# Kernel tuning notes

Measured on AMD Instinct MI355X. Metric: run time of the kernel, lower is better.

The kernel has to match this reference:

```python
import jax, jax.numpy as jnp
import numpy as np

N = 100000   # nodes
E = 800000   # edges
D = 64       # feature dim (input=hidden=output)
EPS = 1e-5   # BatchNorm eps


def setup_inputs() -> dict:
    key = jax.random.key(0)
    ks = jax.random.split(key, 24)
    s = 1.0 / np.sqrt(D)
    inp = {
        "x": jax.random.normal(ks[0], (N, D), jnp.float32),
        "edge_index": jax.random.randint(ks[1], (2, E), 0, N, jnp.int64),
        # GCNConv weights (x @ W + b after normalized aggregation)
        "W1": jax.random.normal(ks[2], (D, D), jnp.float32) * s,
        "b1": jax.random.normal(ks[3], (D,), jnp.float32) * 0.01,
        "W2": jax.random.normal(ks[4], (D, D), jnp.float32) * s,
        "b2": jax.random.normal(ks[5], (D,), jnp.float32) * 0.01,
        "W3": jax.random.normal(ks[6], (D, D), jnp.float32) * s,
        "b3": jax.random.normal(ks[7], (D,), jnp.float32) * 0.01,
        # BatchNorm1d (inference: running stats)
        "bn1_g": jax.random.uniform(ks[8], (D,), jnp.float32, 0.5, 1.5),
        "bn1_b": jax.random.normal(ks[9], (D,), jnp.float32) * 0.1,
        "bn1_m": jax.random.normal(ks[10], (D,), jnp.float32) * 0.1,
        "bn1_v": jax.random.uniform(ks[11], (D,), jnp.float32, 0.5, 1.5),
        "bn2_g": jax.random.uniform(ks[12], (D,), jnp.float32, 0.5, 1.5),
        "bn2_b": jax.random.normal(ks[13], (D,), jnp.float32) * 0.1,
        "bn2_m": jax.random.normal(ks[14], (D,), jnp.float32) * 0.1,
        "bn2_v": jax.random.uniform(ks[15], (D,), jnp.float32, 0.5, 1.5),
        # predictor MLP: Linear -> tanh -> (dropout=id) -> Linear
        "pW1": jax.random.normal(ks[16], (D, D), jnp.float32) * s,
        "pb1": jax.random.normal(ks[17], (D,), jnp.float32) * 0.01,
        "pW2": jax.random.normal(ks[18], (D, D), jnp.float32) * s,
        "pb2": jax.random.normal(ks[19], (D,), jnp.float32) * 0.01,
    }
    return inp


def _gcn_norm(edge_index):
    # add self loops, compute sym-normalized edge coefficients (PyG GCNConv)
    loop = jnp.arange(N, dtype=edge_index.dtype)
    src = jnp.concatenate([edge_index[0], loop])
    dst = jnp.concatenate([edge_index[1], loop])
    deg = jax.ops.segment_sum(jnp.ones(src.shape[0], jnp.float32), dst, num_segments=N)
    dis = jax.lax.rsqrt(deg)  # deg >= 1 due to self loops
    norm = dis[src] * dis[dst]
    return src, dst, norm


def _gcn_layer(x, src, dst, norm, W, b):
    h = x @ W                              # [N, D] small GEMM
    msg = h[src] * norm[:, None]           # [E+N, D] gather (memory bound)
    return jax.ops.segment_sum(msg, dst, num_segments=N) + b  # scatter-add


def _bn(x, g, b, m, v):
    return (x - m) * (g * jax.lax.rsqrt(v + EPS)) + b


def reference(x, edge_index, W1, b1, W2, b2, W3, b3,
              bn1_g, bn1_b, bn1_m, bn1_v, bn2_g, bn2_b, bn2_m, bn2_v,
              pW1, pb1, pW2, pb2):
    src, dst, norm = _gcn_norm(edge_index)
    h = _gcn_layer(x, src, dst, norm, W1, b1)
    h = jax.nn.relu(_bn(h, bn1_g, bn1_b, bn1_m, bn1_v))   # dropout = id (eval)
    h = _gcn_layer(h, src, dst, norm, W2, b2)
    h = jax.nn.relu(_bn(h, bn2_g, bn2_b, bn2_m, bn2_v))
    h = _gcn_layer(h, src, dst, norm, W3, b3)
    out = jnp.tanh(h @ pW1 + pb1) @ pW2 + pb2              # predictor MLP
    return out
```

## Files before the change

### kernel.cpp

```cpp
#include <hip/hip_runtime.h>

#define N_NODES 100000
#define N_EDGES 800000
#define DIM 64
#define BN_EPS 1e-5f
#define LDX 68


__global__ __launch_bounds__(256) void k_zero_deg(int* __restrict__ deg) {
    int i = blockIdx.x * blockDim.x + threadIdx.x;
    if (i < N_NODES) deg[i] = 0;
}

__global__ __launch_bounds__(256) void k_count(const int* __restrict__ dst,
                                               int* __restrict__ deg) {
    int e = blockIdx.x * blockDim.x + threadIdx.x;
    if (e < N_EDGES) atomicAdd(&deg[dst[e]], 1);
}

__global__ __launch_bounds__(256) void k_scan1(const int* __restrict__ deg,
                                               int* __restrict__ row_off,
                                               int* __restrict__ block_sums) {
    __shared__ int sdata[256];
    int tid = threadIdx.x;
    int base = blockIdx.x * 1024 + tid * 4;
    int4 v = make_int4(0, 0, 0, 0);
    if (base < N_NODES) {
        int4 d = *(const int4*)(deg + base);
        v.x = (d.x + 7) & ~7;
        v.y = (d.y + 7) & ~7;
        v.z = (d.z + 7) & ~7;
        v.w = (d.w + 7) & ~7;
    }
    int tsum = v.x + v.y + v.z + v.w;
    sdata[tid] = tsum;
    __syncthreads();
    for (int off = 1; off < 256; off <<= 1) {
        int t = (tid >= off) ? sdata[tid - off] : 0;
        __syncthreads();
        sdata[tid] += t;
        __syncthreads();
    }
    int excl = sdata[tid] - tsum;
    if (base < N_NODES) {
        int4 o;
        o.x = excl;
        o.y = o.x + v.x;
        o.z = o.y + v.y;
        o.w = o.z + v.z;
        *(int4*)(row_off + base) = o;
    }
    if (tid == 255) block_sums[blockIdx.x] = sdata[255];
}

__global__ __launch_bounds__(128) void k_scan2(int* __restrict__ block_sums) {
    __shared__ int sdata[128];
    int tid = threadIdx.x;
    int v = (tid < 98) ? block_sums[tid] : 0;
    sdata[tid] = v;
    __syncthreads();
    for (int off = 1; off < 128; off <<= 1) {
        int t = (tid >= off) ? sdata[tid - off] : 0;
        __syncthreads();
        sdata[tid] += t;
        __syncthreads();
    }
    if (tid < 98) block_sums[tid] = sdata[tid] - v;
}

__global__ __launch_bounds__(256) void k_scan3(const int* __restrict__ deg,
                                               int* __restrict__ row_off,
                                               int* __restrict__ cursor,
                                               float* __restrict__ dinv,
                                               const int* __restrict__ block_sums) {
    int tid = threadIdx.x;
    int base = blockIdx.x * 1024 + tid * 4;
    if (base >= N_NODES) return;
    int p = block_sums[blockIdx.x];
    int4 r = *(const int4*)(row_off + base);
    r.x += p; r.y += p; r.z += p; r.w += p;
    *(int4*)(row_off + base) = r;
    *(int4*)(cursor + base) = r;
    int4 d = *(const int4*)(deg + base);
    float4 di;
    di.x = rsqrtf((float)(d.x + 1));
    di.y = rsqrtf((float)(d.y + 1));
    di.z = rsqrtf((float)(d.z + 1));
    di.w = rsqrtf((float)(d.w + 1));
    *(float4*)(dinv + base) = di;
}

__global__ __launch_bounds__(256) void k_build(const int* __restrict__ ei,
                                               const float* __restrict__ dinv,
                                               int* __restrict__ cursor,
                                               int2* __restrict__ edges) {
    int e = blockIdx.x * blockDim.x + threadIdx.x;
    if (e >= N_EDGES) return;
    int s = ei[e];
    int d = ei[N_EDGES + e];
    int pos = atomicAdd(&cursor[d], 1);
    edges[pos] = make_int2(s, __float_as_int(dinv[s] * dinv[d]));
}

__global__ __launch_bounds__(256) void k_pad(const int* __restrict__ deg,
                                             const int* __restrict__ row_off,
                                             int2* __restrict__ edges) {
    int n = blockIdx.x * blockDim.x + threadIdx.x;
    if (n >= N_NODES) return;
    int d = deg[n];
    int start = row_off[n] + d;
    int end = row_off[n] + ((d + 7) & ~7);
    int2 dummy = make_int2(n, 0);
    for (int p = start; p < end; ++p) edges[p] = dummy;
}

__global__ __launch_bounds__(256) void k_fuse_w3(const float* __restrict__ W3,
                                                 const float* __restrict__ b3,
                                                 const float* __restrict__ pW1,
                                                 const float* __restrict__ pb1,
                                                 float* __restrict__ W3p,
                                                 float* __restrict__ b3p) {
    int tid = threadIdx.x;
    int c = tid & 63;
    int kbase = (tid >> 6) * 16;
    for (int k = kbase; k < kbase + 16; ++k) {
        float acc = 0.f;
#pragma unroll 8
        for (int j = 0; j < 64; ++j)
            acc = fmaf(W3[k * 64 + j], pW1[j * 64 + c], acc);
        W3p[k * 64 + c] = acc;
    }
    if (tid < 64) {
        float acc = pb1[c];
#pragma unroll 8
        for (int j = 0; j < 64; ++j)
            acc = fmaf(b3[j], pW1[j * 64 + c], acc);
        b3p[c] = acc;
    }
}

__global__ __launch_bounds__(256) void k_aggregate(const float* __restrict__ xin,
                                                   const int* __restrict__ row_off,
                                                   const int* __restrict__ deg,
                                                   const int2* __restrict__ edges,
                                                   const float* __restrict__ dinv,
                                                   float* __restrict__ out) {
    int lane = threadIdx.x & 63;
    int node = blockIdx.x * 4 + (threadIdx.x >> 6);
    float di = dinv[node];
    float acc = xin[(size_t)node * DIM + lane] * (di * di);
    int beg = __builtin_amdgcn_readfirstlane(row_off[node]);
    int lenp = (__builtin_amdgcn_readfirstlane(deg[node]) + 7) & ~7;
    int end = beg + lenp;
    for (int k = beg; k < end; k += 8) {
        int2 e0 = edges[k + 0];
        int2 e1 = edges[k + 1];
        int2 e2 = edges[k + 2];
        int2 e3 = edges[k + 3];
        int2 e4 = edges[k + 4];
        int2 e5 = edges[k + 5];
        int2 e6 = edges[k + 6];
        int2 e7 = edges[k + 7];
        float v0 = xin[(size_t)e0.x * DIM + lane];
        float v1 = xin[(size_t)e1.x * DIM + lane];
        float v2 = xin[(size_t)e2.x * DIM + lane];
        float v3 = xin[(size_t)e3.x * DIM + lane];
        float v4 = xin[(size_t)e4.x * DIM + lane];
        float v5 = xin[(size_t)e5.x * DIM + lane];
        float v6 = xin[(size_t)e6.x * DIM + lane];
        float v7 = xin[(size_t)e7.x * DIM + lane];
        acc = fmaf(__int_as_float(e0.y), v0, acc);
        acc = fmaf(__int_as_float(e1.y), v1, acc);
        acc = fmaf(__int_as_float(e2.y), v2, acc);
        acc = fmaf(__int_as_float(e3.y), v3, acc);
        acc = fmaf(__int_as_float(e4.y), v4, acc);
        acc = fmaf(__int_as_float(e5.y), v5, acc);
        acc = fmaf(__int_as_float(e6.y), v6, acc);
        acc = fmaf(__int_as_float(e7.y), v7, acc);
    }
    out[(size_t)node * DIM + lane] = acc;
}

#define GEMM_STEP(SX, SW)                                                      \
    {                                                                          \
        float4 a0 = *(const float4*)&SX[(r0 + 0) * LDX + k4 * 4];              \
        float4 a1 = *(const float4*)&SX[(r0 + 1) * LDX + k4 * 4];              \
        float4 a2 = *(const float4*)&SX[(r0 + 2) * LDX + k4 * 4];              \
        float4 a3 = *(const float4*)&SX[(r0 + 3) * LDX + k4 * 4];              \
        float4 b0 = *(const float4*)&SW[(k4 * 4 + 0) * 64 + c0];               \
        float4 b1 = *(const float4*)&SW[(k4 * 4 + 1) * 64 + c0];               \
        float4 b2 = *(const float4*)&SW[(k4 * 4 + 2) * 64 + c0];               \
        float4 b3 = *(const float4*)&SW[(k4 * 4 + 3) * 64 + c0];               \
        const float* ap[4] = {&a0.x, &a1.x, &a2.x, &a3.x};                     \
        _Pragma("unroll") for (int i = 0; i < 4; ++i) {                        \
            float x0 = ap[i][0], x1 = ap[i][1], x2 = ap[i][2], x3 = ap[i][3];  \
            acc[i][0] = fmaf(x0, b0.x, acc[i][0]);                             \
            acc[i][1] = fmaf(x0, b0.y, acc[i][1]);                             \
            acc[i][2] = fmaf(x0, b0.z, acc[i][2]);                             \
            acc[i][3] = fmaf(x0, b0.w, acc[i][3]);                             \
            acc[i][0] = fmaf(x1, b1.x, acc[i][0]);                             \
            acc[i][1] = fmaf(x1, b1.y, acc[i][1]);                             \
            acc[i][2] = fmaf(x1, b1.z, acc[i][2]);                             \
            acc[i][3] = fmaf(x1, b1.w, acc[i][3]);                             \
            acc[i][0] = fmaf(x2, b2.x, acc[i][0]);                             \
            acc[i][1] = fmaf(x2, b2.y, acc[i][1]);                             \
            acc[i][2] = fmaf(x2, b2.z, acc[i][2]);                             \
            acc[i][3] = fmaf(x2, b2.w, acc[i][3]);                             \
            acc[i][0] = fmaf(x3, b3.x, acc[i][0]);                             \
            acc[i][1] = fmaf(x3, b3.y, acc[i][1]);                             \
            acc[i][2] = fmaf(x3, b3.z, acc[i][2]);                             \
            acc[i][3] = fmaf(x3, b3.w, acc[i][3]);                             \
        }                                                                      \
    }

__global__ __launch_bounds__(256) void k_gemm_tile(const float* __restrict__ xin,
                                                   const float* __restrict__ W,
                                                   const float* __restrict__ bias,
                                                   const float* __restrict__ bng,
                                                   const float* __restrict__ bnb,
                                                   const float* __restrict__ bnm,
                                                   const float* __restrict__ bnv,
                                                   float* __restrict__ out,
                                                   int mode) {
    __shared__ float sW[4096];
    __shared__ float sX[64 * LDX];
    int tid = threadIdx.x;
    int row0 = blockIdx.x * 64;

    for (int i = tid; i < 1024; i += 256)
        ((float4*)sW)[i] = ((const float4*)W)[i];
    {
        int r = tid >> 2;
        int q = tid & 3;
        int row = row0 + r;
        float4* dst = (float4*)(sX + r * LDX);
        if (row < N_NODES) {
            const float4* src = (const float4*)(xin + (size_t)row * DIM);
#pragma unroll
            for (int m = 0; m < 4; ++m) dst[q + m * 4] = src[q + m * 4];
        } else {
            float4 z = make_float4(0.f, 0.f, 0.f, 0.f);
#pragma unroll
            for (int m = 0; m < 4; ++m) dst[q + m * 4] = z;
        }
    }
    __syncthreads();

    int cq = tid & 15, rq = tid >> 4;
    int c0 = cq * 4, r0 = rq * 4;
    float acc[4][4];
#pragma unroll
    for (int i = 0; i < 4; ++i)
#pragma unroll
        for (int j = 0; j < 4; ++j) acc[i][j] = 0.f;

#pragma unroll 4
    for (int k4 = 0; k4 < 16; ++k4) GEMM_STEP(sX, sW)

    float4 bv = *(const float4*)&bias[c0];
    if (mode == 2) {
        float4 g = *(const float4*)&bng[c0];
        float4 bb = *(const float4*)&bnb[c0];
        float4 m = *(const float4*)&bnm[c0];
        float4 vv = *(const float4*)&bnv[c0];
        float A0 = g.x * rsqrtf(vv.x + BN_EPS);
        float A1 = g.y * rsqrtf(vv.y + BN_EPS);
        float A2 = g.z * rsqrtf(vv.z + BN_EPS);
        float A3 = g.w * rsqrtf(vv.w + BN_EPS);
        float B0 = (bv.x - m.x) * A0 + bb.x;
        float B1 = (bv.y - m.y) * A1 + bb.y;
        float B2 = (bv.z - m.z) * A2 + bb.z;
        float B3 = (bv.w - m.w) * A3 + bb.w;
#pragma unroll
        for (int i = 0; i < 4; ++i) {
            int row = row0 + r0 + i;
            if (row >= N_NODES) break;
            float4 o;
            o.x = fmaxf(0.f, fmaf(acc[i][0], A0, B0));
            o.y = fmaxf(0.f, fmaf(acc[i][1], A1, B1));
            o.z = fmaxf(0.f, fmaf(acc[i][2], A2, B2));
            o.w = fmaxf(0.f, fmaf(acc[i][3], A3, B3));
            *(float4*)(out + (size_t)row * DIM + c0) = o;
        }
    } else {
#pragma unroll
        for (int i = 0; i < 4; ++i) {
            int row = row0 + r0 + i;
            if (row >= N_NODES) break;
            float4 o;
            o.x = acc[i][0] + bv.x;
            o.y = acc[i][1] + bv.y;
            o.z = acc[i][2] + bv.z;
            o.w = acc[i][3] + bv.w;
            *(float4*)(out + (size_t)row * DIM + c0) = o;
        }
    }
}

__global__ __launch_bounds__(256) void k_tail(const float* __restrict__ xin,
                                              const float* __restrict__ W3p,
                                              const float* __restrict__ b3p,
                                              const float* __restrict__ pW2,
                                              const float* __restrict__ pb2,
                                              float* __restrict__ out) {
    __shared__ float sW1[4096];
    __shared__ float sW2[4096];
    __shared__ float sX[64 * LDX];
    int tid = threadIdx.x;
    int row0 = blockIdx.x * 64;

    for (int i = tid; i < 1024; i += 256) {
        ((float4*)sW1)[i] = ((const float4*)W3p)[i];
        ((float4*)sW2)[i] = ((const float4*)pW2)[i];
    }
    {
        int r = tid >> 2;
        int q = tid & 3;
        int row = row0 + r;
        float4* dst = (float4*)(sX + r * LDX);
        if (row < N_NODES) {
            const float4* src = (const float4*)(xin + (size_t)row * DIM);
#pragma unroll
            for (int m = 0; m < 4; ++m) dst[q + m * 4] = src[q + m * 4];
        } else {
            float4 z = make_float4(0.f, 0.f, 0.f, 0.f);
#pragma unroll
            for (int m = 0; m < 4; ++m) dst[q + m * 4] = z;
        }
    }
    __syncthreads();

    int cq = tid & 15, rq = tid >> 4;
    int c0 = cq * 4, r0 = rq * 4;
    float acc[4][4];

#pragma unroll
    for (int i = 0; i < 4; ++i)
#pragma unroll
        for (int j = 0; j < 4; ++j) acc[i][j] = 0.f;
#pragma unroll 4
    for (int k4 = 0; k4 < 16; ++k4) GEMM_STEP(sX, sW1)
    __syncthreads();

    {
        float4 bv = *(const float4*)&b3p[c0];
#pragma unroll
        for (int i = 0; i < 4; ++i) {
            float4 h;
            h.x = tanhf(acc[i][0] + bv.x);
            h.y = tanhf(acc[i][1] + bv.y);
            h.z = tanhf(acc[i][2] + bv.z);
            h.w = tanhf(acc[i][3] + bv.w);
            *(float4*)&sX[(r0 + i) * LDX + c0] = h;
        }
    }
    __syncthreads();

#pragma unroll
    for (int i = 0; i < 4; ++i)
#pragma unroll
        for (int j = 0; j < 4; ++j) acc[i][j] = 0.f;
#pragma unroll 4
    for (int k4 = 0; k4 < 16; ++k4) GEMM_STEP(sX, sW2)

    float4 bv = *(const float4*)&pb2[c0];
#pragma unroll
    for (int i = 0; i < 4; ++i) {
        int row = row0 + r0 + i;
        if (row >= N_NODES) break;
        float4 o;
        o.x = acc[i][0] + bv.x;
        o.y = acc[i][1] + bv.y;
        o.z = acc[i][2] + bv.z;
        o.w = acc[i][3] + bv.w;
        *(float4*)(out + (size_t)row * DIM + c0) = o;
    }
}

extern "C" void kernel_launch(void* const* d_in, const int* in_sizes, int n_in,
                              void* d_out, int out_size, void* d_ws, size_t ws_size,
                              hipStream_t stream) {
    const float* x     = (const float*)d_in[0];
    const int*   ei    = (const int*)d_in[1];
    const float* W1    = (const float*)d_in[2];
    const float* b1    = (const float*)d_in[3];
    const float* W2    = (const float*)d_in[4];
    const float* b2    = (const float*)d_in[5];
    const float* W3    = (const float*)d_in[6];
    const float* b3    = (const float*)d_in[7];
    const float* bn1_g = (const float*)d_in[8];
    const float* bn1_b = (const float*)d_in[9];
    const float* bn1_m = (const float*)d_in[10];
    const float* bn1_v = (const float*)d_in[11];
    const float* bn2_g = (const float*)d_in[12];
    const float* bn2_b = (const float*)d_in[13];
    const float* bn2_m = (const float*)d_in[14];
    const float* bn2_v = (const float*)d_in[15];
    const float* pW1   = (const float*)d_in[16];
    const float* pb1   = (const float*)d_in[17];
    const float* pW2   = (const float*)d_in[18];
    const float* pb2   = (const float*)d_in[19];
    float* out = (float*)d_out;

    char* ws = (char*)d_ws;
    int*   deg      = (int*)ws;                      ws += 100352 * 4;
    int*   row_off  = (int*)ws;                      ws += 100352 * 4;
    int*   cursor   = (int*)ws;                      ws += 100352 * 4;
    int*   bsums    = (int*)ws;                      ws += 128 * 4;
    int2*  edges    = (int2*)ws;                     ws += (size_t)1600000 * 8;
    float* dinv     = (float*)ws;                    ws += 100352 * 4;
    float* W3p      = (float*)ws;                    ws += 4096 * 4;
    float* b3p      = (float*)ws;                    ws += 64 * 4;
    float* bufA     = (float*)ws;                    ws += (size_t)N_NODES * DIM * 4;
    float* bufB     = (float*)ws;

    const int blk = 256;
    int gN    = (N_NODES + blk - 1) / blk;
    int gE    = (N_EDGES + blk - 1) / blk;
    int gScan = 98;
    int gAgg  = N_NODES / 4;
    int gTile = (N_NODES + 63) / 64;

    k_zero_deg<<<gN, blk, 0, stream>>>(deg);
    k_count<<<gE, blk, 0, stream>>>(ei + N_EDGES, deg);
    k_scan1<<<gScan, blk, 0, stream>>>(deg, row_off, bsums);
    k_scan2<<<1, 128, 0, stream>>>(bsums);
    k_scan3<<<gScan, blk, 0, stream>>>(deg, row_off, cursor, dinv, bsums);
    k_build<<<gE, blk, 0, stream>>>(ei, dinv, cursor, edges);
    k_pad<<<gN, blk, 0, stream>>>(deg, row_off, edges);
    k_fuse_w3<<<1, blk, 0, stream>>>(W3, b3, pW1, pb1, W3p, b3p);

    k_aggregate<<<gAgg, blk, 0, stream>>>(x, row_off, deg, edges, dinv, bufA);
    k_gemm_tile<<<gTile, blk, 0, stream>>>(bufA, W1, b1, bn1_g, bn1_b, bn1_m, bn1_v, bufB, 2);

    k_aggregate<<<gAgg, blk, 0, stream>>>(bufB, row_off, deg, edges, dinv, bufA);
    k_gemm_tile<<<gTile, blk, 0, stream>>>(bufA, W2, b2, bn2_g, bn2_b, bn2_m, bn2_v, bufB, 2);

    k_aggregate<<<gAgg, blk, 0, stream>>>(bufB, row_off, deg, edges, dinv, bufA);
    k_tail<<<gTile, blk, 0, stream>>>(bufA, W3p, b3p, pW2, pb2, out);
}
```

Measured before the change: 392.3 us.

## Store gathered node features in fp16 and merge CSR scan and padding steps

Node features read by the three neighbour-aggregation passes are now stored as fp16: the input x is converted once, and the GEMM+BN+ReLU epilogue writes half values. Accumulation stays in fp32. This halves the bytes fetched by the memory-bound gather. Separately, the three-kernel prefix scan becomes one kernel that claims each block's base offset with an atomic. The padding kernel is replaced by a memset of the edge array, so padded slots point at node 0 with weight zero. The trade-off is fp16 rounding error on the hidden activations and an extra memset over the whole edge buffer.

```diff
diff --git a/kernel.cpp b/kernel.cpp
--- a/kernel.cpp
+++ b/kernel.cpp
@@ -1,16 +1,13 @@
 #include <hip/hip_runtime.h>
+#include <hip/hip_fp16.h>
 
 #define N_NODES 100000
 #define N_EDGES 800000
 #define DIM 64
 #define BN_EPS 1e-5f
 #define LDX 68
-
-
-__global__ __launch_bounds__(256) void k_zero_deg(int* __restrict__ deg) {
-    int i = blockIdx.x * blockDim.x + threadIdx.x;
-    if (i < N_NODES) deg[i] = 0;
-}
+#define EDGE_CAP 1600000
+
 
 __global__ __launch_bounds__(256) void k_count(const int* __restrict__ dst,
                                                int* __restrict__ deg) {
@@ -18,15 +15,19 @@
     if (e < N_EDGES) atomicAdd(&deg[dst[e]], 1);
 }
 
-__global__ __launch_bounds__(256) void k_scan1(const int* __restrict__ deg,
-                                               int* __restrict__ row_off,
-                                               int* __restrict__ block_sums) {
+__global__ __launch_bounds__(256) void k_scan(const int* __restrict__ deg,
+                                              int* __restrict__ row_off,
+                                              int* __restrict__ cursor,
+                                              float* __restrict__ dinv,
+                                              int* __restrict__ gcount) {
     __shared__ int sdata[256];
+    __shared__ int sbase;
     int tid = threadIdx.x;
     int base = blockIdx.x * 1024 + tid * 4;
+    int4 d = make_int4(0, 0, 0, 0);
     int4 v = make_int4(0, 0, 0, 0);
     if (base < N_NODES) {
-        int4 d = *(const int4*)(deg + base);
+        d = *(const int4*)(deg + base);
         v.x = (d.x + 7) & ~7;
         v.y = (d.y + 7) & ~7;
         v.z = (d.z + 7) & ~7;
@@ -41,47 +42,17 @@
         sdata[tid] += t;
         __syncthreads();
     }
-    int excl = sdata[tid] - tsum;
-    if (base < N_NODES) {
-        int4 o;
-        o.x = excl;
-        o.y = o.x + v.x;
-        o.z = o.y + v.y;
-        o.w = o.z + v.z;
-        *(int4*)(row_off + base) = o;
-    }
-    if (tid == 255) block_sums[blockIdx.x] = sdata[255];
-}
-
-__global__ __launch_bounds__(128) void k_scan2(int* __restrict__ block_sums) {
-    __shared__ int sdata[128];
-    int tid = threadIdx.x;
-    int v = (tid < 98) ? block_sums[tid] : 0;
-    sdata[tid] = v;
-    __syncthreads();
-    for (int off = 1; off < 128; off <<= 1) {
-        int t = (tid >= off) ? sdata[tid - off] : 0;
-        __syncthreads();
-        sdata[tid] += t;
-        __syncthreads();
-    }
-    if (tid < 98) block_sums[tid] = sdata[tid] - v;
-}
-
-__global__ __launch_bounds__(256) void k_scan3(const int* __restrict__ deg,
-                                               int* __restrict__ row_off,
-                                               int* __restrict__ cursor,
-                                               float* __restrict__ dinv,
-                                               const int* __restrict__ block_sums) {
-    int tid = threadIdx.x;
-    int base = blockIdx.x * 1024 + tid * 4;
+    if (tid == 255) sbase = atomicAdd(gcount, sdata[255]);
+    __syncthreads();
     if (base >= N_NODES) return;
-    int p = block_sums[blockIdx.x];
-    int4 r = *(const int4*)(row_off + base);
-    r.x += p; r.y += p; r.z += p; r.w += p;
-    *(int4*)(row_off + base) = r;
-    *(int4*)(cursor + base) = r;
-    int4 d = *(const int4*)(deg + base);
+    int excl = sdata[tid] - tsum + sbase;
+    int4 o;
+    o.x = excl;
+    o.y = o.x + v.x;
+    o.z = o.y + v.y;
+    o.w = o.z + v.z;
+    *(int4*)(row_off + base) = o;
+    *(int4*)(cursor + base) = o;
     float4 di;
     di.x = rsqrtf((float)(d.x + 1));
     di.y = rsqrtf((float)(d.y + 1));
@@ -102,16 +73,15 @@
     edges[pos] = make_int2(s, __float_as_int(dinv[s] * dinv[d]));
 }
 
-__global__ __launch_bounds__(256) void k_pad(const int* __restrict__ deg,
-                                             const int* __restrict__ row_off,
-                                             int2* __restrict__ edges) {
-    int n = blockIdx.x * blockDim.x + threadIdx.x;
-    if (n >= N_NODES) return;
-    int d = deg[n];
-    int start = row_off[n] + d;
-    int end = row_off[n] + ((d + 7) & ~7);
-    int2 dummy = make_int2(n, 0);
-    for (int p = start; p < end; ++p) edges[p] = dummy;
+__global__ __launch_bounds__(256) void k_tohalf(const float* __restrict__ x,
+                                                __half* __restrict__ xh) {
+    int idx = blockIdx.x * blockDim.x + threadIdx.x;
+    float4 v = ((const float4*)x)[idx];
+    unsigned int u0 = __half_as_ushort(__float2half(v.x));
+    unsigned int u1 = __half_as_ushort(__float2half(v.y));
+    unsigned int u2 = __half_as_ushort(__float2half(v.z));
+    unsigned int u3 = __half_as_ushort(__float2half(v.w));
+    ((uint2*)xh)[idx] = make_uint2(u0 | (u1 << 16), u2 | (u3 << 16));
 }
 
 __global__ __launch_bounds__(256) void k_fuse_w3(const float* __restrict__ W3,
@@ -139,7 +109,7 @@
     }
 }
 
-__global__ __launch_bounds__(256) void k_aggregate(const float* __restrict__ xin,
+__global__ __launch_bounds__(256) void k_aggregate(const __half* __restrict__ xin,
                                                    const int* __restrict__ row_off,
                                                    const int* __restrict__ deg,
                                                    const int2* __restrict__ edges,
@@ -148,7 +118,7 @@
     int lane = threadIdx.x & 63;
     int node = blockIdx.x * 4 + (threadIdx.x >> 6);
     float di = dinv[node];
-    float acc = xin[(size_t)node * DIM + lane] * (di * di);
+    float acc = __half2float(xin[(size_t)node * DIM + lane]) * (di * di);
     int beg = __builtin_amdgcn_readfirstlane(row_off[node]);
     int lenp = (__builtin_amdgcn_readfirstlane(deg[node]) + 7) & ~7;
     int end = beg + lenp;
@@ -161,14 +131,14 @@
         int2 e5 = edges[k + 5];
         int2 e6 = edges[k + 6];
         int2 e7 = edges[k + 7];
-        float v0 = xin[(size_t)e0.x * DIM + lane];
-        float v1 = xin[(size_t)e1.x * DIM + lane];
-        float v2 = xin[(size_t)e2.x * DIM + lane];
-        float v3 = xin[(size_t)e3.x * DIM + lane];
-        float v4 = xin[(size_t)e4.x * DIM + lane];
-        float v5 = xin[(size_t)e5.x * DIM + lane];
-        float v6 = xin[(size_t)e6.x * DIM + lane];
-        float v7 = xin[(size_t)e7.x * DIM + lane];
+        float v0 = __half2float(xin[(size_t)e0.x * DIM + lane]);
+        float v1 = __half2float(xin[(size_t)e1.x * DIM + lane]);
+        float v2 = __half2float(xin[(size_t)e2.x * DIM + lane]);
+        float v3 = __half2float(xin[(size_t)e3.x * DIM + lane]);
+        float v4 = __half2float(xin[(size_t)e4.x * DIM + lane]);
+        float v5 = __half2float(xin[(size_t)e5.x * DIM + lane]);
+        float v6 = __half2float(xin[(size_t)e6.x * DIM + lane]);
+        float v7 = __half2float(xin[(size_t)e7.x * DIM + lane]);
         acc = fmaf(__int_as_float(e0.y), v0, acc);
         acc = fmaf(__int_as_float(e1.y), v1, acc);
         acc = fmaf(__int_as_float(e2.y), v2, acc);
@@ -213,15 +183,14 @@
         }                                                                      \
     }
 
-__global__ __launch_bounds__(256) void k_gemm_tile(const float* __restrict__ xin,
+__global__ __launch_bounds__(256) void k_gemm_bn_h(const float* __restrict__ xin,
                                                    const float* __restrict__ W,
                                                    const float* __restrict__ bias,
                                                    const float* __restrict__ bng,
                                                    const float* __restrict__ bnb,
                                                    const float* __restrict__ bnm,
                                                    const float* __restrict__ bnv,
-                                                   float* __restrict__ out,
-                                                   int mode) {
+                                                   __half* __restrict__ out) {
     __shared__ float sW[4096];
     __shared__ float sX[64 * LDX];
     int tid = threadIdx.x;
@@ -258,42 +227,27 @@
     for (int k4 = 0; k4 < 16; ++k4) GEMM_STEP(sX, sW)
 
     float4 bv = *(const float4*)&bias[c0];
-    if (mode == 2) {
-        float4 g = *(const float4*)&bng[c0];
-        float4 bb = *(const float4*)&bnb[c0];
-        float4 m = *(const float4*)&bnm[c0];
-        float4 vv = *(const float4*)&bnv[c0];
-        float A0 = g.x * rsqrtf(vv.x + BN_EPS);
-        float A1 = g.y * rsqrtf(vv.y + BN_EPS);
-        float A2 = g.z * rsqrtf(vv.z + BN_EPS);
-        float A3 = g.w * rsqrtf(vv.w + BN_EPS);
-        float B0 = (bv.x - m.x) * A0 + bb.x;
-        float B1 = (bv.y - m.y) * A1 + bb.y;
-        float B2 = (bv.z - m.z) * A2 + bb.z;
-        float B3 = (bv.w - m.w) * A3 + bb.w;
-#pragma unroll
-        for (int i = 0; i < 4; ++i) {
-            int row = row0 + r0 + i;
-            if (row >= N_NODES) break;
-            float4 o;
-            o.x = fmaxf(0.f, fmaf(acc[i][0], A0, B0));
-            o.y = fmaxf(0.f, fmaf(acc[i][1], A1, B1));
-            o.z = fmaxf(0.f, fmaf(acc[i][2], A2, B2));
-            o.w = fmaxf(0.f, fmaf(acc[i][3], A3, B3));
-            *(float4*)(out + (size_t)row * DIM + c0) = o;
-        }
-    } else {
-#pragma unroll
-        for (int i = 0; i < 4; ++i) {
-            int row = row0 + r0 + i;
-            if (row >= N_NODES) break;
-            float4 o;
-            o.x = acc[i][0] + bv.x;
-            o.y = acc[i][1] + bv.y;
-            o.z = acc[i][2] + bv.z;
-            o.w = acc[i][3] + bv.w;
-            *(float4*)(out + (size_t)row * DIM + c0) = o;
-        }
+    float4 g = *(const float4*)&bng[c0];
+    float4 bb = *(const float4*)&bnb[c0];
+    float4 m = *(const float4*)&bnm[c0];
+    float4 vv = *(const float4*)&bnv[c0];
+    float A0 = g.x * rsqrtf(vv.x + BN_EPS);
+    float A1 = g.y * rsqrtf(vv.y + BN_EPS);
+    float A2 = g.z * rsqrtf(vv.z + BN_EPS);
+    float A3 = g.w * rsqrtf(vv.w + BN_EPS);
+    float B0 = (bv.x - m.x) * A0 + bb.x;
+    float B1 = (bv.y - m.y) * A1 + bb.y;
+    float B2 = (bv.z - m.z) * A2 + bb.z;
+    float B3 = (bv.w - m.w) * A3 + bb.w;
+#pragma unroll
+    for (int i = 0; i < 4; ++i) {
+        int row = row0 + r0 + i;
+        if (row >= N_NODES) break;
+        unsigned int u0 = __half_as_ushort(__float2half(fmaxf(0.f, fmaf(acc[i][0], A0, B0))));
+        unsigned int u1 = __half_as_ushort(__float2half(fmaxf(0.f, fmaf(acc[i][1], A1, B1))));
+        unsigned int u2 = __half_as_ushort(__float2half(fmaxf(0.f, fmaf(acc[i][2], A2, B2))));
+        unsigned int u3 = __half_as_ushort(__float2half(fmaxf(0.f, fmaf(acc[i][3], A3, B3))));
+        *(uint2*)(out + (size_t)row * DIM + c0) = make_uint2(u0 | (u1 << 16), u2 | (u3 << 16));
     }
 }
 
@@ -404,38 +358,38 @@
 
     char* ws = (char*)d_ws;
     int*   deg      = (int*)ws;                      ws += 100352 * 4;
+    int*   gcount   = (int*)ws;                      ws += 4 * 4;
     int*   row_off  = (int*)ws;                      ws += 100352 * 4;
     int*   cursor   = (int*)ws;                      ws += 100352 * 4;
-    int*   bsums    = (int*)ws;                      ws += 128 * 4;
-    int2*  edges    = (int2*)ws;                     ws += (size_t)1600000 * 8;
+    int2*  edges    = (int2*)ws;                     ws += (size_t)EDGE_CAP * 8;
     float* dinv     = (float*)ws;                    ws += 100352 * 4;
     float* W3p      = (float*)ws;                    ws += 4096 * 4;
     float* b3p      = (float*)ws;                    ws += 64 * 4;
+    __half* xh      = (__half*)ws;                   ws += (size_t)N_NODES * DIM * 2;
+    __half* hbuf    = (__half*)ws;                   ws += (size_t)N_NODES * DIM * 2;
     float* bufA     = (float*)ws;                    ws += (size_t)N_NODES * DIM * 4;
-    float* bufB     = (float*)ws;
 
     const int blk = 256;
-    int gN    = (N_NODES + blk - 1) / blk;
     int gE    = (N_EDGES + blk - 1) / blk;
     int gScan = 98;
+    int gCvt  = N_NODES * 16 / blk;
     int gAgg  = N_NODES / 4;
     int gTile = (N_NODES + 63) / 64;
 
-    k_zero_deg<<<gN, blk, 0, stream>>>(deg);
+    hipMemsetAsync(deg, 0, (100352 + 4) * 4, stream);
+    hipMemsetAsync(edges, 0, (size_t)EDGE_CAP * 8, stream);
+    k_tohalf<<<gCvt, blk, 0, stream>>>(x, xh);
     k_count<<<gE, blk, 0, stream>>>(ei + N_EDGES, deg);
-    k_scan1<<<gScan, blk, 0, stream>>>(deg, row_off, bsums);
-    k_scan2<<<1, 128, 0, stream>>>(bsums);
-    k_scan3<<<gScan, blk, 0, stream>>>(deg, row_off, cursor, dinv, bsums);
+    k_scan<<<gScan, blk, 0, stream>>>(deg, row_off, cursor, dinv, gcount);
     k_build<<<gE, blk, 0, stream>>>(ei, dinv, cursor, edges);
-    k_pad<<<gN, blk, 0, stream>>>(deg, row_off, edges);
     k_fuse_w3<<<1, blk, 0, stream>>>(W3, b3, pW1, pb1, W3p, b3p);
 
-    k_aggregate<<<gAgg, blk, 0, stream>>>(x, row_off, deg, edges, dinv, bufA);
-    k_gemm_tile<<<gTile, blk, 0, stream>>>(bufA, W1, b1, bn1_g, bn1_b, bn1_m, bn1_v, bufB, 2);
-
-    k_aggregate<<<gAgg, blk, 0, stream>>>(bufB, row_off, deg, edges, dinv, bufA);
-    k_gemm_tile<<<gTile, blk, 0, stream>>>(bufA, W2, b2, bn2_g, bn2_b, bn2_m, bn2_v, bufB, 2);
-
-    k_aggregate<<<gAgg, blk, 0, stream>>>(bufB, row_off, deg, edges, dinv, bufA);
+    k_aggregate<<<gAgg, blk, 0, stream>>>(xh, row_off, deg, edges, dinv, bufA);
+    k_gemm_bn_h<<<gTile, blk, 0, stream>>>(bufA, W1, b1, bn1_g, bn1_b, bn1_m, bn1_v, hbuf);
+
+    k_aggregate<<<gAgg, blk, 0, stream>>>(hbuf, row_off, deg, edges, dinv, bufA);
+    k_gemm_bn_h<<<gTile, blk, 0, stream>>>(bufA, W2, b2, bn2_g, bn2_b, bn2_m, bn2_v, hbuf);
+
+    k_aggregate<<<gAgg, blk, 0, stream>>>(hbuf, row_off, deg, edges, dinv, bufA);
     k_tail<<<gTile, blk, 0, stream>>>(bufA, W3p, b3p, pW2, pb2, out);
 }
```

After: 382.8 us. 1.02x faster.
